# Performance work log

Measured on AMD Instinct MI355X. Metric: run time of the kernel, lower is better.

Reference implementation:

```python
import jax, jax.numpy as jnp
import numpy as np
from jax import lax

Q = 16384      # num questions (hyperedges)
S = 16384      # num students (nodes)
F = 64         # feat_dim
EMB = 64       # emb_dim
H = 32         # student_hist_max
C = 16384      # student_attn_chunk_size
E = 393216     # incidence edges per channel (24 chunks)


def setup_inputs() -> dict:
    key = jax.random.key(0)
    ks = jax.random.split(key, 24)
    rn = lambda k, sh, s=1.0: jax.random.normal(k, sh, dtype=jnp.float32) * s
    ri = lambda k, sh, hi: jax.random.randint(k, sh, 0, hi, dtype=jnp.int32)
    return {
        'x': rn(ks[0], (Q, F)),
        's_emb': rn(ks[1], (S, F)),
        'W_Q': rn(ks[2], (2 * F, F), 0.05), 'b_Q': jnp.zeros((F,), jnp.float32),
        'W_K': rn(ks[3], (F, F), 0.05),     'b_K': jnp.zeros((F,), jnp.float32),
        'W_V': rn(ks[4], (F, F), 0.05),     'b_V': jnp.zeros((F,), jnp.float32),
        'W_fuse': rn(ks[5], (2 * F, F), 0.05), 'b_fuse': jnp.zeros((F,), jnp.float32),
        'W_K2': rn(ks[6], (F, F), 0.05),    'b_K2': jnp.zeros((F,), jnp.float32),
        'W_V2': rn(ks[7], (F, F), 0.05),    'b_V2': jnp.zeros((F,), jnp.float32),
        'W_proj': rn(ks[8], (2 * F, EMB), 0.05), 'b_proj': jnp.zeros((EMB,), jnp.float32),
        'h1_bias': jnp.zeros((2, F), jnp.float32),  # nn.init.zeros_ in source
        'h2_bias': jnp.zeros((2, F), jnp.float32),
        'hist_qid_pos': ri(ks[9], (S, H), Q),
        'hist_cnt_pos': ri(ks[10], (S,), H + 1),
        'hist_qid_neg': ri(ks[11], (S, H), Q),
        'hist_cnt_neg': ri(ks[12], (S,), H + 1),
        'edge_sid_pos': ri(ks[13], (E,), S),
        'edge_qid_pos': ri(ks[14], (E,), Q),
        'edge_sid_neg': ri(ks[15], (E,), S),
        'edge_qid_neg': ri(ks[16], (E,), Q),
    }


def reference(x, s_emb, W_Q, b_Q, W_K, b_K, W_V, b_V, W_fuse, b_fuse,
              W_K2, b_K2, W_V2, b_V2, W_proj, b_proj, h1_bias, h2_bias,
              hist_qid_pos, hist_cnt_pos, hist_qid_neg, hist_cnt_neg,
              edge_sid_pos, edge_qid_pos, edge_sid_neg, edge_qid_neg):
    scale = jnp.float32(1.0 / np.sqrt(F))
    NEG = jnp.float32(-1e9)

    def channel(hist_qid, hist_cnt, e_sid, e_qid, ch):
        # dense per-student history keys/values: [S, H, F]
        xh = x[hist_qid]
        Kh = xh @ W_K + b_K + h1_bias[ch]
        Vh = xh @ W_V + b_V
        mask = jnp.arange(H, dtype=jnp.int32)[None, :] < hist_cnt[:, None]  # [S,H]

        def chunk_fn(args):
            sid, qid = args  # [C]
            # edge-level query: W_Q([x_q || e_u])
            q = jnp.concatenate([x[qid], s_emb[sid]], axis=-1) @ W_Q + b_Q  # [C,F]
            sc = jnp.einsum('cf,chf->ch', q, Kh[sid]) * scale               # [C,H]
            m = mask[sid]
            a = jax.nn.softmax(jnp.where(m, sc, NEG), axis=-1)
            a = jnp.where(m, a, 0.0)  # empty history -> zero output
            return jnp.einsum('ch,chf->cf', a, Vh[sid])                     # [C,F]

        nchunks = E // C
        agg = lax.map(chunk_fn, (e_sid.reshape(nchunks, C), e_qid.reshape(nchunks, C)))
        agg = agg.reshape(E, F)
        # fuse student embedding with history-aggregated context
        s_repr = jnp.concatenate([s_emb[e_sid], agg], axis=-1) @ W_fuse + b_fuse  # [E,F]
        # hop 2: question attends over its member students (segment softmax over e_qid)
        k2 = s_repr @ W_K2 + b_K2 + h2_bias[ch]
        v2 = s_repr @ W_V2 + b_V2
        sc2 = jnp.sum(x[e_qid] * k2, axis=-1) * scale                      # [E]
        mx = jax.ops.segment_max(sc2, e_qid, num_segments=Q)
        ex = jnp.exp(sc2 - mx[e_qid])
        den = jax.ops.segment_sum(ex, e_qid, num_segments=Q)
        alpha = ex / jnp.maximum(den[e_qid], 1e-9)
        return jax.ops.segment_sum(alpha[:, None] * v2, e_qid, num_segments=Q)  # [Q,F]

    pos = channel(hist_qid_pos, hist_cnt_pos, edge_sid_pos, edge_qid_pos, 0)
    neg = channel(hist_qid_neg, hist_cnt_neg, edge_sid_neg, edge_qid_neg, 1)
    return jnp.concatenate([pos, neg], axis=-1) @ W_proj + b_proj  # [Q, EMB]
```

## Files before the change

kernel.cpp:

```cpp
#include <hip/hip_runtime.h>

typedef float v2f __attribute__((ext_vector_type(2)));
typedef float v4f __attribute__((ext_vector_type(4)));

#define QN 16384
#define SN 16384
#define HN 32
#define EN 393216
#define KPAD 68
#define CAP 64

__global__ __launch_bounds__(256) void prep_kernel(
    const float* __restrict__ x, const float* __restrict__ s_emb,
    const float* __restrict__ W_Q, const float* __restrict__ b_Q,
    const float* __restrict__ W_K, const float* __restrict__ b_K,
    const float* __restrict__ W_V, const float* __restrict__ b_V,
    const float* __restrict__ W_fuse, const float* __restrict__ b_fuse,
    const float* __restrict__ W_K2, const float* __restrict__ b_K2,
    const float* __restrict__ h1b, const float* __restrict__ h2b,
    const int* __restrict__ es_pos, const int* __restrict__ eq_pos,
    const int* __restrict__ es_neg, const int* __restrict__ eq_neg,
    float* __restrict__ xKpos, float* __restrict__ xKneg,
    float* __restrict__ xVfp, float* __restrict__ xQ1, float* __restrict__ xq2p,
    float* __restrict__ c2pos, float* __restrict__ c2neg,
    float* __restrict__ sQ, float* __restrict__ sfp,
    int* __restrict__ cnt_pos, int* __restrict__ cnt_neg,
    int* __restrict__ csr_pos, int* __restrict__ csr_neg)
{
  __shared__ float xs[512];
  __shared__ float vs[512];
  __shared__ float wk2t[64 * 66];
  const int bid = blockIdx.x;
  const int t = threadIdx.x;
  const int j = t & 31, r = t >> 5;

  if (bid < 2048) {
    const int q = bid * 8 + r;
    if (t < 128) *(v4f*)&xs[t * 4] = *(const v4f*)&x[bid * 512 + t * 4];
    for (int i = 0; i < 16; i++) {
      int idx = i * 256 + t;
      wk2t[(idx & 63) * 66 + (idx >> 6)] = W_K2[idx];
    }
    __syncthreads();

    v2f accK = *(const v2f*)&b_K[2 * j];
    v2f accV = *(const v2f*)&b_V[2 * j];
    v2f accQ = {0.f, 0.f};
    float a2x = 0.f, a2y = 0.f;
    for (int g = 0; g < 64; g++) {
      float xv = xs[r * 64 + g];
      accK += xv * *(const v2f*)&W_K[g * 64 + 2 * j];
      accV += xv * *(const v2f*)&W_V[g * 64 + 2 * j];
      accQ += xv * *(const v2f*)&W_Q[g * 64 + 2 * j];
      a2x += xv * wk2t[g * 66 + j];
      a2y += xv * wk2t[g * 66 + j + 32];
    }
    *(v2f*)&xKpos[q * 64 + 2 * j] = accK + *(const v2f*)&h1b[2 * j];
    *(v2f*)&xKneg[q * 64 + 2 * j] = accK + *(const v2f*)&h1b[64 + 2 * j];
    *(v2f*)&xQ1[q * 64 + 2 * j] = accQ;
    v2f a2 = {a2x, a2y};
    *(v2f*)&xq2p[q * 64 + 2 * j] = a2;
    *(v2f*)&vs[r * 64 + 2 * j] = accV;

    v2f xv2 = *(const v2f*)&xs[r * 64 + 2 * j];
    v2f bb0 = *(const v2f*)&b_K2[2 * j] + *(const v2f*)&h2b[2 * j];
    v2f bb1 = *(const v2f*)&b_K2[2 * j] + *(const v2f*)&h2b[64 + 2 * j];
    v2f t0 = xv2 * bb0, t1 = xv2 * bb1;
    float p0 = t0.x + t0.y, p1v = t1.x + t1.y;
    for (int k = 16; k >= 1; k >>= 1) {
      p0 += __shfl_xor(p0, k, 32);
      p1v += __shfl_xor(p1v, k, 32);
    }
    if (j == 0) { c2pos[q] = p0 * 0.125f; c2neg[q] = p1v * 0.125f; }

    __syncthreads();
    float vfx = 0.f, vfy = 0.f;
    for (int g = 0; g < 64; g++) {
      float vv = vs[r * 64 + g];
      vfx += vv * W_fuse[(64 + g) * 64 + j];
      vfy += vv * W_fuse[(64 + g) * 64 + j + 32];
    }
    v2f vf = {vfx, vfy};
    *(v2f*)&xVfp[q * 64 + 2 * j] = vf;
  } else if (bid < 4096) {
    const int b2 = bid - 2048;
    const int s = b2 * 8 + r;
    if (t < 128) *(v4f*)&xs[t * 4] = *(const v4f*)&s_emb[b2 * 512 + t * 4];
    __syncthreads();
    v2f aq = *(const v2f*)&b_Q[2 * j];
    float afx = b_fuse[j], afy = b_fuse[j + 32];
    for (int g = 0; g < 64; g++) {
      float v = xs[r * 64 + g];
      aq += v * *(const v2f*)&W_Q[(64 + g) * 64 + 2 * j];
      afx += v * W_fuse[g * 64 + j];
      afy += v * W_fuse[g * 64 + j + 32];
    }
    *(v2f*)&sQ[s * 64 + 2 * j] = aq;
    v2f af = {afx, afy};
    *(v2f*)&sfp[s * 64 + 2 * j] = af;
  } else {
    const int hb = bid - 4096;
    const bool neg = hb >= 1536;
    const int* __restrict__ sid = neg ? es_neg : es_pos;
    const int* __restrict__ qid = neg ? eq_neg : eq_pos;
    int* __restrict__ cnt = neg ? cnt_neg : cnt_pos;
    int* __restrict__ csr = neg ? csr_neg : csr_pos;
    const int i = (neg ? hb - 1536 : hb) * 256 + t;
    const int s = sid[i];
    const int slot = atomicAdd(&cnt[s], 1);
    if (slot < CAP) csr[s * CAP + slot] = qid[i];
  }
}

#define LDBATCH(BASE, Q0,Q1,Q2,Q3, A0,A1,A2,A3, X0,X1,X2,X3, C0,C1,C2,C3) do { \
    int _m = ne - 1; \
    Q0 = csr[ebeg + (BASE)]; \
    Q1 = csr[ebeg + min((BASE) + 1, _m)]; \
    Q2 = csr[ebeg + min((BASE) + 2, _m)]; \
    Q3 = csr[ebeg + min((BASE) + 3, _m)]; \
    A0 = *(const v2f*)&xQ1[(size_t)Q0 * 64 + 2 * c] + sqv; \
    A1 = *(const v2f*)&xQ1[(size_t)Q1 * 64 + 2 * c] + sqv; \
    A2 = *(const v2f*)&xQ1[(size_t)Q2 * 64 + 2 * c] + sqv; \
    A3 = *(const v2f*)&xQ1[(size_t)Q3 * 64 + 2 * c] + sqv; \
    X0 = *(const v2f*)&xq2p[(size_t)Q0 * 64 + 2 * c]; \
    X1 = *(const v2f*)&xq2p[(size_t)Q1 * 64 + 2 * c]; \
    X2 = *(const v2f*)&xq2p[(size_t)Q2 * 64 + 2 * c]; \
    X3 = *(const v2f*)&xq2p[(size_t)Q3 * 64 + 2 * c]; \
    C0 = c2[Q0]; C1 = c2[Q1]; C2 = c2[Q2]; C3 = c2[Q3]; \
  } while (0)

__global__ __launch_bounds__(256, 5) void main_kernel(
    const float* __restrict__ xKpos, const float* __restrict__ xKneg,
    const float* __restrict__ xVfp, const float* __restrict__ xQ1,
    const float* __restrict__ xq2p,
    const float* __restrict__ c2pos, const float* __restrict__ c2neg,
    const float* __restrict__ sQ, const float* __restrict__ sfp,
    const int* __restrict__ hq_pos, const int* __restrict__ hc_pos,
    const int* __restrict__ hq_neg, const int* __restrict__ hc_neg,
    const int* __restrict__ cnt_pos, const int* __restrict__ csr_pos,
    const int* __restrict__ cnt_neg, const int* __restrict__ csr_neg,
    float* __restrict__ num_pos, float* __restrict__ den_pos,
    float* __restrict__ num_neg, float* __restrict__ den_neg)
{
  const int s = blockIdx.x;
  const int ch = blockIdx.y;
  const float* __restrict__ xK = ch ? xKneg : xKpos;
  const float* __restrict__ c2 = ch ? c2neg : c2pos;
  const int* __restrict__ hq = ch ? hq_neg : hq_pos;
  const int* __restrict__ hc = ch ? hc_neg : hc_pos;
  const int* __restrict__ cntS = ch ? cnt_neg : cnt_pos;
  const int* __restrict__ csr = ch ? csr_neg : csr_pos;
  float* __restrict__ num = ch ? num_neg : num_pos;
  float* __restrict__ den = ch ? den_neg : den_pos;

  const int t = threadIdx.x;
  __shared__ float Kl[HN * KPAD];
  __shared__ float Vl[HN * 64];
  __shared__ float Qg[8 * 4 * 64];
  __shared__ float Al[8 * 32 * 4];
  __shared__ int hql[HN];

  const int hcnt = hc[s];
  if (t < HN) hql[t] = hq[s * HN + t];
  __syncthreads();
  for (int i = 0; i < 2; i++) {
    int idx = i * 256 + t;
    int h = idx >> 4, jj = idx & 15;
    int row = hql[h];
    *(v4f*)&Kl[h * KPAD + jj * 4] = *(const v4f*)&xK[(size_t)row * 64 + jj * 4];
    *(v4f*)&Vl[h * 64 + jj * 4] = *(const v4f*)&xVfp[(size_t)row * 64 + jj * 4];
  }
  const int ebeg = s * CAP;
  const int ne = min(cntS[s], CAP);
  __syncthreads();

  const float scale = 0.125f;
  const int g = t >> 5;
  const int c = t & 31;
  float* __restrict__ Qb = &Qg[g * 256];
  float* __restrict__ Ab = &Al[g * 128];
  const v4f* kp = (const v4f*)&Kl[c * KPAD];
  const v2f sqv = *(const v2f*)&sQ[(size_t)s * 64 + 2 * c];
  const v2f sfv = *(const v2f*)&sfp[(size_t)s * 64 + 2 * c];

  int i0 = g * 4;
  if (i0 < ne) {
    int q0, q1, q2, q3;
    v2f a0, a1, a2, a3, x20, x21, x22, x23;
    float cc0, cc1, cc2, cc3;
    LDBATCH(i0, q0, q1, q2, q3, a0, a1, a2, a3, x20, x21, x22, x23, cc0, cc1, cc2, cc3);

    for (; i0 < ne; i0 += 32) {
      const int nb = ne - i0;
      *(v2f*)&Qb[2 * c] = a0;
      *(v2f*)&Qb[64 + 2 * c] = a1;
      *(v2f*)&Qb[128 + 2 * c] = a2;
      *(v2f*)&Qb[192 + 2 * c] = a3;

      int n0, n1, n2, n3;
      v2f na0, na1, na2, na3, nx0, nx1, nx2, nx3;
      float nc0, nc1, nc2, nc3;
      const bool more = (i0 + 32) < ne;
      if (more) {
        LDBATCH(i0 + 32, n0, n1, n2, n3, na0, na1, na2, na3,
                nx0, nx1, nx2, nx3, nc0, nc1, nc2, nc3);
      }

      v2f ac0 = {0.f, 0.f}, ac1 = {0.f, 0.f}, ac2 = {0.f, 0.f}, ac3 = {0.f, 0.f};
#pragma unroll 4
      for (int k = 0; k < 16; k++) {
        v4f k4 = kp[k];
        v4f qa = ((const v4f*)&Qb[0])[k];
        ac0 += qa.lo * k4.lo; ac0 += qa.hi * k4.hi;
        v4f qb = ((const v4f*)&Qb[64])[k];
        ac1 += qb.lo * k4.lo; ac1 += qb.hi * k4.hi;
        v4f qc = ((const v4f*)&Qb[128])[k];
        ac2 += qc.lo * k4.lo; ac2 += qc.hi * k4.hi;
        v4f qd = ((const v4f*)&Qb[192])[k];
        ac3 += qd.lo * k4.lo; ac3 += qd.hi * k4.hi;
      }
      float s0 = ac0.x + ac0.y, s1 = ac1.x + ac1.y;
      float s2 = ac2.x + ac2.y, s3 = ac3.x + ac3.y;
      const bool valid = (c < hcnt);
      float e0 = valid ? __expf(s0 * scale) : 0.f;
      float e1 = valid ? __expf(s1 * scale) : 0.f;
      float e2 = valid ? __expf(s2 * scale) : 0.f;
      float e3 = valid ? __expf(s3 * scale) : 0.f;
      float d0 = e0, d1 = e1, d2 = e2, d3 = e3;
      for (int k = 16; k >= 1; k >>= 1) {
        d0 += __shfl_xor(d0, k, 32);
        d1 += __shfl_xor(d1, k, 32);
        d2 += __shfl_xor(d2, k, 32);
        d3 += __shfl_xor(d3, k, 32);
      }
      v4f av;
      av.x = (d0 > 0.f) ? e0 / d0 : 0.f;
      av.y = (d1 > 0.f) ? e1 / d1 : 0.f;
      av.z = (d2 > 0.f) ? e2 / d2 : 0.f;
      av.w = (d3 > 0.f) ? e3 / d3 : 0.f;
      *(v4f*)&Ab[c * 4] = av;

      v2f r0 = sfv, r1 = sfv, r2 = sfv, r3 = sfv;
#pragma unroll 8
      for (int h = 0; h < HN; h++) {
        v2f vv = *(const v2f*)&Vl[h * 64 + 2 * c];
        v4f a4 = *(const v4f*)&Ab[h * 4];
        r0 += a4.x * vv;
        r1 += a4.y * vv;
        r2 += a4.z * vv;
        r3 += a4.w * vv;
      }

      float p0 = r0.x * x20.x + r0.y * x20.y;
      float p1 = r1.x * x21.x + r1.y * x21.y;
      float p2 = r2.x * x22.x + r2.y * x22.y;
      float p3 = r3.x * x23.x + r3.y * x23.y;
      for (int k = 16; k >= 1; k >>= 1) {
        p0 += __shfl_xor(p0, k, 32);
        p1 += __shfl_xor(p1, k, 32);
        p2 += __shfl_xor(p2, k, 32);
        p3 += __shfl_xor(p3, k, 32);
      }
      float ew0 = __expf(p0 * scale + cc0);
      float ew1 = __expf(p1 * scale + cc1);
      float ew2 = __expf(p2 * scale + cc2);
      float ew3 = __expf(p3 * scale + cc3);

      atomicAdd(&num[(size_t)q0 * 64 + c], ew0 * r0.x);
      atomicAdd(&num[(size_t)q0 * 64 + 32 + c], ew0 * r0.y);
      if (nb > 1) {
        atomicAdd(&num[(size_t)q1 * 64 + c], ew1 * r1.x);
        atomicAdd(&num[(size_t)q1 * 64 + 32 + c], ew1 * r1.y);
      }
      if (nb > 2) {
        atomicAdd(&num[(size_t)q2 * 64 + c], ew2 * r2.x);
        atomicAdd(&num[(size_t)q2 * 64 + 32 + c], ew2 * r2.y);
      }
      if (nb > 3) {
        atomicAdd(&num[(size_t)q3 * 64 + c], ew3 * r3.x);
        atomicAdd(&num[(size_t)q3 * 64 + 32 + c], ew3 * r3.y);
      }
      if (c < min(nb, 4)) {
        int qd = (c == 0) ? q0 : (c == 1) ? q1 : (c == 2) ? q2 : q3;
        float ed = (c == 0) ? ew0 : (c == 1) ? ew1 : (c == 2) ? ew2 : ew3;
        atomicAdd(&den[qd], ed);
      }

      q0 = n0; q1 = n1; q2 = n2; q3 = n3;
      a0 = na0; a1 = na1; a2 = na2; a3 = na3;
      x20 = nx0; x21 = nx1; x22 = nx2; x23 = nx3;
      cc0 = nc0; cc1 = nc1; cc2 = nc2; cc3 = nc3;
    }
  }
}

__global__ __launch_bounds__(256) void final_kernel(
    const float* __restrict__ num_pos, const float* __restrict__ den_pos,
    const float* __restrict__ num_neg, const float* __restrict__ den_neg,
    const float* __restrict__ W_V2, const float* __restrict__ b_V2,
    const float* __restrict__ W_proj, const float* __restrict__ b_proj,
    float* __restrict__ out)
{
  __shared__ float np[8 * 64], nn[8 * 64], hp[8 * 64], hn[8 * 64];
  int t = threadIdx.x;
  int j = t & 31, r = t >> 5;
  int q = blockIdx.x * 8 + r;
  if (t < 128) {
    *(v4f*)&np[t * 4] = *(const v4f*)&num_pos[blockIdx.x * 512 + t * 4];
    *(v4f*)&nn[t * 4] = *(const v4f*)&num_neg[blockIdx.x * 512 + t * 4];
  }
  __syncthreads();
  float dp = den_pos[q], dn = den_neg[q];
  float ip = (dp > 0.f) ? 1.f / dp : 0.f;
  float in_ = (dn > 0.f) ? 1.f / dn : 0.f;
  v2f zero = {0.f, 0.f};
  v2f bv = *(const v2f*)&b_V2[2 * j];
  v2f hpv = (dp > 0.f) ? bv : zero;
  v2f hnv = (dn > 0.f) ? bv : zero;
  for (int f = 0; f < 64; f++) {
    v2f w = *(const v2f*)&W_V2[f * 64 + 2 * j];
    hpv += (np[r * 64 + f] * ip) * w;
    hnv += (nn[r * 64 + f] * in_) * w;
  }
  *(v2f*)&hp[r * 64 + 2 * j] = hpv;
  *(v2f*)&hn[r * 64 + 2 * j] = hnv;
  __syncthreads();
  v2f o = *(const v2f*)&b_proj[2 * j];
  for (int f = 0; f < 64; f++) {
    o += hp[r * 64 + f] * *(const v2f*)&W_proj[f * 64 + 2 * j];
    o += hn[r * 64 + f] * *(const v2f*)&W_proj[(64 + f) * 64 + 2 * j];
  }
  *(v2f*)&out[q * 64 + 2 * j] = o;
}

extern "C" void kernel_launch(void* const* d_in, const int* in_sizes, int n_in,
                              void* d_out, int out_size, void* d_ws, size_t ws_size,
                              hipStream_t stream) {
  const float* x      = (const float*)d_in[0];
  const float* s_emb  = (const float*)d_in[1];
  const float* W_Q    = (const float*)d_in[2];
  const float* b_Q    = (const float*)d_in[3];
  const float* W_K    = (const float*)d_in[4];
  const float* b_K    = (const float*)d_in[5];
  const float* W_V    = (const float*)d_in[6];
  const float* b_V    = (const float*)d_in[7];
  const float* W_fuse = (const float*)d_in[8];
  const float* b_fuse = (const float*)d_in[9];
  const float* W_K2   = (const float*)d_in[10];
  const float* b_K2   = (const float*)d_in[11];
  const float* W_V2   = (const float*)d_in[12];
  const float* b_V2   = (const float*)d_in[13];
  const float* W_proj = (const float*)d_in[14];
  const float* b_proj = (const float*)d_in[15];
  const float* h1b    = (const float*)d_in[16];
  const float* h2b    = (const float*)d_in[17];
  const int* hq_pos   = (const int*)d_in[18];
  const int* hc_pos   = (const int*)d_in[19];
  const int* hq_neg   = (const int*)d_in[20];
  const int* hc_neg   = (const int*)d_in[21];
  const int* es_pos   = (const int*)d_in[22];
  const int* eq_pos   = (const int*)d_in[23];
  const int* es_neg   = (const int*)d_in[24];
  const int* eq_neg   = (const int*)d_in[25];
  float* out = (float*)d_out;

  size_t off = 0;
  char* base = (char*)d_ws;
  auto carve = [&](size_t bytes) -> void* {
    void* p = base + off;
    off += (bytes + 255) & ~(size_t)255;
    return p;
  };
  float* num_pos = (float*)carve((size_t)QN * 64 * 4);
  float* num_neg = (float*)carve((size_t)QN * 64 * 4);
  float* den_pos = (float*)carve((size_t)QN * 4);
  float* den_neg = (float*)carve((size_t)QN * 4);
  int* cnt_pos   = (int*)carve((size_t)SN * 4);
  int* cnt_neg   = (int*)carve((size_t)SN * 4);
  size_t zero_bytes = off;
  float* xKpos = (float*)carve((size_t)QN * 64 * 4);
  float* xKneg = (float*)carve((size_t)QN * 64 * 4);
  float* xVfp  = (float*)carve((size_t)QN * 64 * 4);
  float* xQ1   = (float*)carve((size_t)QN * 64 * 4);
  float* xq2p  = (float*)carve((size_t)QN * 64 * 4);
  float* sQ    = (float*)carve((size_t)SN * 64 * 4);
  float* sfp   = (float*)carve((size_t)SN * 64 * 4);
  float* c2pos = (float*)carve((size_t)QN * 4);
  float* c2neg = (float*)carve((size_t)QN * 4);
  int* csr_pos = (int*)carve((size_t)SN * CAP * 4);
  int* csr_neg = (int*)carve((size_t)SN * CAP * 4);
  if (off > ws_size) return;

  hipMemsetAsync(d_ws, 0, zero_bytes, stream);

  prep_kernel<<<4096 + 2 * (EN / 256), 256, 0, stream>>>(
      x, s_emb, W_Q, b_Q, W_K, b_K, W_V, b_V, W_fuse, b_fuse, W_K2, b_K2,
      h1b, h2b, es_pos, eq_pos, es_neg, eq_neg,
      xKpos, xKneg, xVfp, xQ1, xq2p, c2pos, c2neg, sQ, sfp,
      cnt_pos, cnt_neg, csr_pos, csr_neg);

  main_kernel<<<dim3(SN, 2), 256, 0, stream>>>(
      xKpos, xKneg, xVfp, xQ1, xq2p, c2pos, c2neg, sQ, sfp,
      hq_pos, hc_pos, hq_neg, hc_neg,
      cnt_pos, csr_pos, cnt_neg, csr_neg,
      num_pos, den_pos, num_neg, den_neg);

  final_kernel<<<QN / 8, 256, 0, stream>>>(num_pos, den_pos, num_neg, den_neg,
                                           W_V2, b_V2, W_proj, b_proj, out);
}
```

Measured before the change: 612.0 us.

## Privatize scatter accumulators per XCD with workgroup-scope atomics, reduce in final kernel

Gives each XCD its own copy of the num/den accumulators, selected by reading the hardware XCC_ID register, and switches the scatter atomics to workgroup-scope relaxed atomics so they can resolve in the XCD-local L2 instead of going device-coherent. The final kernel then sums the eight partial copies before normalization. The change also restructures the per-edge dot-product accumulation and the den atomics into per-slot blocks. The trade-off is eight times the accumulator memory, a larger memset, and extra reads in the final kernel. Correctness relies on workgroup-scope atomics staying coherent among blocks on the same XCD, which holds only if those atomics are serviced at the shared L2.

```diff
diff --git a/kernel.cpp b/kernel.cpp
--- a/kernel.cpp
+++ b/kernel.cpp
@@ -9,6 +9,7 @@
 #define EN 393216
 #define KPAD 68
 #define CAP 64
+#define NXCD 8
 
 __global__ __launch_bounds__(256) void prep_kernel(
     const float* __restrict__ x, const float* __restrict__ s_emb,
@@ -139,8 +140,9 @@
     const int* __restrict__ hq_neg, const int* __restrict__ hc_neg,
     const int* __restrict__ cnt_pos, const int* __restrict__ csr_pos,
     const int* __restrict__ cnt_neg, const int* __restrict__ csr_neg,
-    float* __restrict__ num_pos, float* __restrict__ den_pos,
-    float* __restrict__ num_neg, float* __restrict__ den_neg)
+    float* __restrict__ numC_pos, float* __restrict__ denC_pos,
+    float* __restrict__ numC_neg, float* __restrict__ denC_neg,
+    int multi)
 {
   const int s = blockIdx.x;
   const int ch = blockIdx.y;
@@ -150,8 +152,14 @@
   const int* __restrict__ hc = ch ? hc_neg : hc_pos;
   const int* __restrict__ cntS = ch ? cnt_neg : cnt_pos;
   const int* __restrict__ csr = ch ? csr_neg : csr_pos;
-  float* __restrict__ num = ch ? num_neg : num_pos;
-  float* __restrict__ den = ch ? den_neg : den_pos;
+
+  int xcd = 0;
+  if (multi) {
+    asm volatile("s_getreg_b32 %0, hwreg(HW_REG_XCC_ID)" : "=s"(xcd));
+    xcd &= (NXCD - 1);
+  }
+  float* __restrict__ num = (ch ? numC_neg : numC_pos) + (size_t)xcd * (QN * 64);
+  float* __restrict__ den = (ch ? denC_neg : denC_pos) + (size_t)xcd * QN;
 
   const int t = threadIdx.x;
   __shared__ float Kl[HN * KPAD];
@@ -183,6 +191,11 @@
   const v2f sqv = *(const v2f*)&sQ[(size_t)s * 64 + 2 * c];
   const v2f sfv = *(const v2f*)&sfp[(size_t)s * 64 + 2 * c];
 
+  auto atomAdd = [&](float* p, float v) {
+    if (multi) __hip_atomic_fetch_add(p, v, __ATOMIC_RELAXED, __HIP_MEMORY_SCOPE_WORKGROUP);
+    else atomicAdd(p, v);
+  };
+
   int i0 = g * 4;
   if (i0 < ne) {
     int q0, q1, q2, q3;
@@ -206,21 +219,19 @@
                 nx0, nx1, nx2, nx3, nc0, nc1, nc2, nc3);
       }
 
-      v2f ac0 = {0.f, 0.f}, ac1 = {0.f, 0.f}, ac2 = {0.f, 0.f}, ac3 = {0.f, 0.f};
+      float s0 = 0.f, s1 = 0.f, s2 = 0.f, s3 = 0.f;
 #pragma unroll 4
       for (int k = 0; k < 16; k++) {
         v4f k4 = kp[k];
         v4f qa = ((const v4f*)&Qb[0])[k];
-        ac0 += qa.lo * k4.lo; ac0 += qa.hi * k4.hi;
+        s0 += qa.x * k4.x + qa.y * k4.y + qa.z * k4.z + qa.w * k4.w;
         v4f qb = ((const v4f*)&Qb[64])[k];
-        ac1 += qb.lo * k4.lo; ac1 += qb.hi * k4.hi;
+        s1 += qb.x * k4.x + qb.y * k4.y + qb.z * k4.z + qb.w * k4.w;
         v4f qc = ((const v4f*)&Qb[128])[k];
-        ac2 += qc.lo * k4.lo; ac2 += qc.hi * k4.hi;
+        s2 += qc.x * k4.x + qc.y * k4.y + qc.z * k4.z + qc.w * k4.w;
         v4f qd = ((const v4f*)&Qb[192])[k];
-        ac3 += qd.lo * k4.lo; ac3 += qd.hi * k4.hi;
-      }
-      float s0 = ac0.x + ac0.y, s1 = ac1.x + ac1.y;
-      float s2 = ac2.x + ac2.y, s3 = ac3.x + ac3.y;
+        s3 += qd.x * k4.x + qd.y * k4.y + qd.z * k4.z + qd.w * k4.w;
+      }
       const bool valid = (c < hcnt);
       float e0 = valid ? __expf(s0 * scale) : 0.f;
       float e1 = valid ? __expf(s1 * scale) : 0.f;
@@ -251,39 +262,37 @@
         r3 += a4.w * vv;
       }
 
-      float p0 = r0.x * x20.x + r0.y * x20.y;
-      float p1 = r1.x * x21.x + r1.y * x21.y;
-      float p2 = r2.x * x22.x + r2.y * x22.y;
-      float p3 = r3.x * x23.x + r3.y * x23.y;
-      for (int k = 16; k >= 1; k >>= 1) {
-        p0 += __shfl_xor(p0, k, 32);
-        p1 += __shfl_xor(p1, k, 32);
-        p2 += __shfl_xor(p2, k, 32);
-        p3 += __shfl_xor(p3, k, 32);
-      }
-      float ew0 = __expf(p0 * scale + cc0);
-      float ew1 = __expf(p1 * scale + cc1);
-      float ew2 = __expf(p2 * scale + cc2);
-      float ew3 = __expf(p3 * scale + cc3);
-
-      atomicAdd(&num[(size_t)q0 * 64 + c], ew0 * r0.x);
-      atomicAdd(&num[(size_t)q0 * 64 + 32 + c], ew0 * r0.y);
+      {
+        float p = r0.x * x20.x + r0.y * x20.y;
+        for (int k = 16; k >= 1; k >>= 1) p += __shfl_xor(p, k, 32);
+        float ew = __expf(p * scale + cc0);
+        atomAdd(&num[(size_t)q0 * 64 + c], ew * r0.x);
+        atomAdd(&num[(size_t)q0 * 64 + 32 + c], ew * r0.y);
+        if (c == 0) atomAdd(&den[q0], ew);
+      }
       if (nb > 1) {
-        atomicAdd(&num[(size_t)q1 * 64 + c], ew1 * r1.x);
-        atomicAdd(&num[(size_t)q1 * 64 + 32 + c], ew1 * r1.y);
+        float p = r1.x * x21.x + r1.y * x21.y;
+        for (int k = 16; k >= 1; k >>= 1) p += __shfl_xor(p, k, 32);
+        float ew = __expf(p * scale + cc1);
+        atomAdd(&num[(size_t)q1 * 64 + c], ew * r1.x);
+        atomAdd(&num[(size_t)q1 * 64 + 32 + c], ew * r1.y);
+        if (c == 0) atomAdd(&den[q1], ew);
       }
       if (nb > 2) {
-        atomicAdd(&num[(size_t)q2 * 64 + c], ew2 * r2.x);
-        atomicAdd(&num[(size_t)q2 * 64 + 32 + c], ew2 * r2.y);
+        float p = r2.x * x22.x + r2.y * x22.y;
+        for (int k = 16; k >= 1; k >>= 1) p += __shfl_xor(p, k, 32);
+        float ew = __expf(p * scale + cc2);
+        atomAdd(&num[(size_t)q2 * 64 + c], ew * r2.x);
+        atomAdd(&num[(size_t)q2 * 64 + 32 + c], ew * r2.y);
+        if (c == 0) atomAdd(&den[q2], ew);
       }
       if (nb > 3) {
-        atomicAdd(&num[(size_t)q3 * 64 + c], ew3 * r3.x);
-        atomicAdd(&num[(size_t)q3 * 64 + 32 + c], ew3 * r3.y);
-      }
-      if (c < min(nb, 4)) {
-        int qd = (c == 0) ? q0 : (c == 1) ? q1 : (c == 2) ? q2 : q3;
-        float ed = (c == 0) ? ew0 : (c == 1) ? ew1 : (c == 2) ? ew2 : ew3;
-        atomicAdd(&den[qd], ed);
+        float p = r3.x * x23.x + r3.y * x23.y;
+        for (int k = 16; k >= 1; k >>= 1) p += __shfl_xor(p, k, 32);
+        float ew = __expf(p * scale + cc3);
+        atomAdd(&num[(size_t)q3 * 64 + c], ew * r3.x);
+        atomAdd(&num[(size_t)q3 * 64 + 32 + c], ew * r3.y);
+        if (c == 0) atomAdd(&den[q3], ew);
       }
 
       q0 = n0; q1 = n1; q2 = n2; q3 = n3;
@@ -295,8 +304,9 @@
 }
 
 __global__ __launch_bounds__(256) void final_kernel(
-    const float* __restrict__ num_pos, const float* __restrict__ den_pos,
-    const float* __restrict__ num_neg, const float* __restrict__ den_neg,
+    const float* __restrict__ numC_pos, const float* __restrict__ denC_pos,
+    const float* __restrict__ numC_neg, const float* __restrict__ denC_neg,
+    int nc,
     const float* __restrict__ W_V2, const float* __restrict__ b_V2,
     const float* __restrict__ W_proj, const float* __restrict__ b_proj,
     float* __restrict__ out)
@@ -306,11 +316,20 @@
   int j = t & 31, r = t >> 5;
   int q = blockIdx.x * 8 + r;
   if (t < 128) {
-    *(v4f*)&np[t * 4] = *(const v4f*)&num_pos[blockIdx.x * 512 + t * 4];
-    *(v4f*)&nn[t * 4] = *(const v4f*)&num_neg[blockIdx.x * 512 + t * 4];
+    v4f ap = {0.f, 0.f, 0.f, 0.f}, an = {0.f, 0.f, 0.f, 0.f};
+    for (int x = 0; x < nc; x++) {
+      ap += *(const v4f*)&numC_pos[(size_t)x * QN * 64 + blockIdx.x * 512 + t * 4];
+      an += *(const v4f*)&numC_neg[(size_t)x * QN * 64 + blockIdx.x * 512 + t * 4];
+    }
+    *(v4f*)&np[t * 4] = ap;
+    *(v4f*)&nn[t * 4] = an;
   }
   __syncthreads();
-  float dp = den_pos[q], dn = den_neg[q];
+  float dp = 0.f, dn = 0.f;
+  for (int x = 0; x < nc; x++) {
+    dp += denC_pos[(size_t)x * QN + q];
+    dn += denC_neg[(size_t)x * QN + q];
+  }
   float ip = (dp > 0.f) ? 1.f / dp : 0.f;
   float in_ = (dn > 0.f) ? 1.f / dn : 0.f;
   v2f zero = {0.f, 0.f};
@@ -364,6 +383,20 @@
   const int* eq_neg   = (const int*)d_in[25];
   float* out = (float*)d_out;
 
+  auto layout_bytes = [](int nc) -> size_t {
+    auto al = [](size_t b) { return (b + 255) & ~(size_t)255; };
+    size_t z = 0;
+    z += al((size_t)nc * QN * 64 * 4) * 2;
+    z += al((size_t)nc * QN * 4) * 2;
+    z += al((size_t)SN * 4) * 2;
+    size_t nz = al((size_t)QN * 64 * 4) * 5
+              + al((size_t)SN * 64 * 4) * 2
+              + al((size_t)QN * 4) * 2
+              + al((size_t)SN * CAP * 4) * 2;
+    return z + nz;
+  };
+  const int NC = (layout_bytes(NXCD) <= ws_size) ? NXCD : 1;
+
   size_t off = 0;
   char* base = (char*)d_ws;
   auto carve = [&](size_t bytes) -> void* {
@@ -371,12 +404,12 @@
     off += (bytes + 255) & ~(size_t)255;
     return p;
   };
-  float* num_pos = (float*)carve((size_t)QN * 64 * 4);
-  float* num_neg = (float*)carve((size_t)QN * 64 * 4);
-  float* den_pos = (float*)carve((size_t)QN * 4);
-  float* den_neg = (float*)carve((size_t)QN * 4);
-  int* cnt_pos   = (int*)carve((size_t)SN * 4);
-  int* cnt_neg   = (int*)carve((size_t)SN * 4);
+  float* numC_pos = (float*)carve((size_t)NC * QN * 64 * 4);
+  float* numC_neg = (float*)carve((size_t)NC * QN * 64 * 4);
+  float* denC_pos = (float*)carve((size_t)NC * QN * 4);
+  float* denC_neg = (float*)carve((size_t)NC * QN * 4);
+  int* cnt_pos    = (int*)carve((size_t)SN * 4);
+  int* cnt_neg    = (int*)carve((size_t)SN * 4);
   size_t zero_bytes = off;
   float* xKpos = (float*)carve((size_t)QN * 64 * 4);
   float* xKneg = (float*)carve((size_t)QN * 64 * 4);
@@ -403,8 +436,8 @@
       xKpos, xKneg, xVfp, xQ1, xq2p, c2pos, c2neg, sQ, sfp,
       hq_pos, hc_pos, hq_neg, hc_neg,
       cnt_pos, csr_pos, cnt_neg, csr_neg,
-      num_pos, den_pos, num_neg, den_neg);
-
-  final_kernel<<<QN / 8, 256, 0, stream>>>(num_pos, den_pos, num_neg, den_neg,
-                                           W_V2, b_V2, W_proj, b_proj, out);
+      numC_pos, denC_pos, numC_neg, denC_neg, (NC == NXCD) ? 1 : 0);
+
+  final_kernel<<<QN / 8, 256, 0, stream>>>(numC_pos, denC_pos, numC_neg, denC_neg,
+                                           NC, W_V2, b_V2, W_proj, b_proj, out);
 }
```

Measured after the change: 617.0 us. About the same (+0.8%).
